# Performance work log

Measured on AMD Instinct MI355X. Metric: run time of the kernel, lower is better.

Reference implementation:

```python
import jax, jax.numpy as jnp
import numpy as np

N_USERS = 100000
M_ITEMS = 200000
K_DIM = 128
N_BASKET = 50
GAMMA = (1.0, 1.0, 1.0, 1.0)


def setup_inputs() -> dict:
    key = jax.random.key(0)
    k1, k2, k3, k4, k5 = jax.random.split(key, 5)
    n, m, k = N_USERS, M_ITEMS, K_DIM
    p = n + 2 * m
    # Build one transaction x of length 2*p: [target transaction t | t^m transaction]
    rng = np.random.default_rng(0)
    x = np.zeros(2 * p, dtype=np.float32)
    # target transaction t
    x[rng.integers(n)] = 1.0                      # user one-hot
    x[n + rng.integers(m)] = 1.0                  # target item one-hot
    basket = rng.choice(m, size=N_BASKET, replace=False)
    x[n + m + basket] = 1.0                       # basket multi-hot
    # t^m transaction (unused by forward math, present for faithfulness)
    x[p + rng.integers(n)] = 1.0
    x[p + n + rng.integers(m)] = 1.0
    basket2 = rng.choice(m, size=N_BASKET, replace=False)
    x[p + n + m + basket2] = 1.0
    return {
        "x": jnp.asarray(x),
        "delta": jnp.ones((1,), dtype=jnp.float32),
        "pmi": jnp.zeros((1,), dtype=jnp.float32),
        "w_0": jax.random.normal(k1, (1,), dtype=jnp.float32),
        "w_bias": jax.random.normal(k2, (p, 1), dtype=jnp.float32),
        "u_V": jax.random.normal(k3, (n, k), dtype=jnp.float32),
        "t_V": jax.random.normal(k4, (m, k), dtype=jnp.float32),
        "b_V": jax.random.normal(k5, (m, k), dtype=jnp.float32),
    }


def _fm(t, w_0, w_bias, u_V, t_V, b_V):
    n, m = u_V.shape[0], t_V.shape[0]
    xr = t[None, :]                                  # (1, n+2m)
    bias = xr @ w_bias                               # (1, 1)
    u_vec = xr[:, :n] @ u_V                          # (1, k) user latent
    t_vec = xr[:, n:n + m] @ t_V                     # (1, k) target-item latent
    xb = t[n + m:]                                   # (m,) basket multi-hot mask
    s = xb @ b_V                                     # (k,)  sum of selected basket vecs
    sq_sum = jnp.sum(xb @ (b_V * b_V))               # scalar sum_i ||b_i||^2
    u_t = jnp.sum(u_vec * t_vec, axis=-1, keepdims=True)   # (1,1)
    t_b = jnp.sum(t_vec * s, axis=-1, keepdims=True)        # (1,1) sum_i t.b_i
    # closed-form FM pairwise trick: sum_{i<j} b_i.b_j = 0.5*(||sum||^2 - sum ||.||^2)
    bs = 0.5 * (jnp.sum(s * s) - sq_sum)                    # scalar
    u_b = jnp.sum(u_vec * s, axis=-1, keepdims=True)        # (1,1)
    g0, g1, g2, g3 = GAMMA
    return w_0 + bias + g0 * u_t + g1 * t_b + g2 * bs + g3 * u_b


def reference(x, delta, pmi, w_0, w_bias, u_V, t_V, b_V):
    n, m = u_V.shape[0], t_V.shape[0]
    p = n + 2 * m
    t = x[:p]
    y = _fm(t, w_0, w_bias, u_V, t_V, b_V)           # (1,1)
    y = -jax.nn.log_sigmoid(y * delta)
    return y
```

## Files before the change

### kernel.cpp

```cpp
#include <hip/hip_runtime.h>
#include <math.h>

#define N_USERS 100000
#define M_ITEMS 200000
#define K_DIM   128
#define P_DIM   (N_USERS + 2 * M_ITEMS)
#define N4      (P_DIM / 4)
#define SCAN_T  256
#define SCAN_BLOCKS ((N4 + SCAN_T - 1) / SCAN_T)
#define SLOTS   64
#define MAXNZ   256


__global__ __launch_bounds__(SCAN_T) void scan_kernel(
        const float* __restrict__ x,
        int* __restrict__ counts,
        int* __restrict__ gidx,
        float* __restrict__ gval) {
    __shared__ int lc;
    __shared__ int   lidx[SLOTS];
    __shared__ float lval[SLOTS];
    const int tid = threadIdx.x;
    const int b   = blockIdx.x;
    if (tid == 0) lc = 0;
    __syncthreads();

    const int i4 = b * SCAN_T + tid;
    if (i4 < N4) {
        float4 v = reinterpret_cast<const float4*>(x)[i4];
        float a[4] = {v.x, v.y, v.z, v.w};
        #pragma unroll
        for (int j = 0; j < 4; ++j) {
            if (a[j] != 0.0f) {
                int p = atomicAdd(&lc, 1);
                if (p < SLOTS) { lidx[p] = 4 * i4 + j; lval[p] = a[j]; }
            }
        }
    }
    __syncthreads();
    int c = lc; if (c > SLOTS) c = SLOTS;
    if (tid == 0) counts[b] = c;
    if (tid < c) {
        gidx[b * SLOTS + tid] = lidx[tid];
        gval[b * SLOTS + tid] = lval[tid];
    }
}

__global__ __launch_bounds__(1024) void finish_kernel(
        const int* __restrict__ counts,
        const int* __restrict__ gidx,
        const float* __restrict__ gval,
        const float* __restrict__ w0,
        const float* __restrict__ delta,
        const float* __restrict__ w_bias,
        const float* __restrict__ uV,
        const float* __restrict__ tV,
        const float* __restrict__ bV,
        float* __restrict__ out) {
    const int tid = threadIdx.x;

    __shared__ int   lcnt;
    __shared__ int   lidx[MAXNZ];
    __shared__ float lval[MAXNZ];
    __shared__ float sb[MAXNZ];
    __shared__ float pu[8][K_DIM], pt[8][K_DIM], ps[8][K_DIM], psq[8][K_DIM];
    __shared__ float red[5][K_DIM];

    if (tid == 0) lcnt = 0;
    __syncthreads();

    if (tid < SCAN_BLOCKS) {
        int cb = counts[tid];
        for (int j = 0; j < cb; ++j) {
            int p = atomicAdd(&lcnt, 1);
            if (p < MAXNZ) {
                lidx[p] = gidx[tid * SLOTS + j];
                lval[p] = gval[tid * SLOTS + j];
            }
        }
    }
    __syncthreads();
    int cnt = lcnt; if (cnt > MAXNZ) cnt = MAXNZ;

    if (tid < MAXNZ)
        sb[tid] = (tid < cnt) ? lval[tid] * w_bias[lidx[tid]] : 0.0f;

    const int k  = tid & (K_DIM - 1);
    const int sl = tid >> 7;
    float u = 0.0f, t = 0.0f, s = 0.0f, sq = 0.0f;
    for (int e = sl; e < cnt; e += 8) {
        const int   idx = lidx[e];
        const float val = lval[e];
        if (idx < N_USERS) {
            u += val * uV[(size_t)idx * K_DIM + k];
        } else if (idx < N_USERS + M_ITEMS) {
            t += val * tV[(size_t)(idx - N_USERS) * K_DIM + k];
        } else {
            float b = bV[(size_t)(idx - N_USERS - M_ITEMS) * K_DIM + k];
            s  += val * b;
            sq += val * b * b;
        }
    }
    pu[sl][k] = u; pt[sl][k] = t; ps[sl][k] = s; psq[sl][k] = sq;
    __syncthreads();

    if (tid < K_DIM) {
        float U = 0.0f, T = 0.0f, S = 0.0f, SQ = 0.0f;
        #pragma unroll
        for (int j = 0; j < 8; ++j) {
            U += pu[j][tid]; T += pt[j][tid]; S += ps[j][tid]; SQ += psq[j][tid];
        }
        red[0][tid] = U * T;
        red[1][tid] = T * S;
        red[2][tid] = S * S;
        red[3][tid] = U * S;
        red[4][tid] = SQ;
    }
    __syncthreads();
    if (tid < 128) sb[tid] += sb[tid + 128];
    __syncthreads();
    for (int off = K_DIM / 2; off > 0; off >>= 1) {
        if (tid < off) {
            #pragma unroll
            for (int j = 0; j < 5; ++j) red[j][tid] += red[j][tid + off];
            sb[tid] += sb[tid + off];
        }
        __syncthreads();
    }

    if (tid == 0) {
        const float ut = red[0][0], tb = red[1][0], ss = red[2][0],
                    ub = red[3][0], sqs = red[4][0];
        const float bs = 0.5f * (ss - sqs);
        float y = w0[0] + sb[0] + ut + tb + bs + ub;
        float z = y * delta[0];
        float a = -z;
        out[0] = fmaxf(a, 0.0f) + log1pf(expf(-fabsf(a)));
    }
}

extern "C" void kernel_launch(void* const* d_in, const int* in_sizes, int n_in,
                              void* d_out, int out_size, void* d_ws, size_t ws_size,
                              hipStream_t stream) {
    const float* x      = (const float*)d_in[0];
    const float* delta  = (const float*)d_in[1];
    const float* w0     = (const float*)d_in[3];
    const float* w_bias = (const float*)d_in[4];
    const float* uV     = (const float*)d_in[5];
    const float* tV     = (const float*)d_in[6];
    const float* bV     = (const float*)d_in[7];
    float* out = (float*)d_out;

    int*   counts = (int*)d_ws;
    int*   gidx   = (int*)((char*)d_ws + 4096);
    float* gval   = (float*)((char*)d_ws + 4096 + SCAN_BLOCKS * SLOTS * sizeof(int));

    scan_kernel<<<SCAN_BLOCKS, SCAN_T, 0, stream>>>(x, counts, gidx, gval);
    finish_kernel<<<1, 1024, 0, stream>>>(counts, gidx, gval, w0, delta,
                                          w_bias, uV, tV, bV, out);
}
```

Before: 206.9 us.

## Fuse scan and finish kernels via last-block ticket and batch row loads

Merges the two launches into one kernel: each 1024-thread block compacts its nonzeros, then an atomic ticket picks the last block to finish, which does the gather and reduction. The scan block size grows from 256 to 1024 threads, so there are fewer per-block slot lists to merge, and MAXNZ shrinks to 128. The gather loop now issues up to 16 row loads per thread up front before accumulating, to expose memory-level parallelism. This removes a kernel launch and the gap between launches. In exchange it relies on a persistent global ticket taken modulo the block count, and the fixed 16-per-slice and 128-entry caps limit how many nonzeros it can handle.

```diff
diff --git a/kernel.cpp b/kernel.cpp
--- a/kernel.cpp
+++ b/kernel.cpp
@@ -6,26 +6,43 @@
 #define K_DIM   128
 #define P_DIM   (N_USERS + 2 * M_ITEMS)
 #define N4      (P_DIM / 4)
-#define SCAN_T  256
-#define SCAN_BLOCKS ((N4 + SCAN_T - 1) / SCAN_T)
+#define BLK     1024
+#define NBLK    ((N4 + BLK - 1) / BLK)
 #define SLOTS   64
-#define MAXNZ   256
+#define MAXNZ   128
 
 
-__global__ __launch_bounds__(SCAN_T) void scan_kernel(
+__device__ unsigned int g_ticket;
+
+__global__ __launch_bounds__(BLK) void fused_kernel(
         const float* __restrict__ x,
-        int* __restrict__ counts,
-        int* __restrict__ gidx,
-        float* __restrict__ gval) {
-    __shared__ int lc;
+        int*   __restrict__ counts,
+        int*   __restrict__ gidx,
+        float* __restrict__ gval,
+        const float* __restrict__ w0,
+        const float* __restrict__ delta,
+        const float* __restrict__ w_bias,
+        const float* __restrict__ uV,
+        const float* __restrict__ tV,
+        const float* __restrict__ bV,
+        float* __restrict__ out) {
+    __shared__ int   lc;
     __shared__ int   lidx[SLOTS];
     __shared__ float lval[SLOTS];
+    __shared__ int   is_last;
+    __shared__ int   lcnt;
+    __shared__ int   fidx[MAXNZ];
+    __shared__ float fval[MAXNZ];
+    __shared__ float sb[MAXNZ];
+    __shared__ float pu[8][K_DIM], pt[8][K_DIM], ps[8][K_DIM], psq[8][K_DIM];
+    __shared__ float red[5][K_DIM];
+
     const int tid = threadIdx.x;
     const int b   = blockIdx.x;
     if (tid == 0) lc = 0;
     __syncthreads();
 
-    const int i4 = b * SCAN_T + tid;
+    const int i4 = b * BLK + tid;
     if (i4 < N4) {
         float4 v = reinterpret_cast<const float4*>(x)[i4];
         float a[4] = {v.x, v.y, v.z, v.w};
@@ -44,38 +61,24 @@
         gidx[b * SLOTS + tid] = lidx[tid];
         gval[b * SLOTS + tid] = lval[tid];
     }
-}
 
-__global__ __launch_bounds__(1024) void finish_kernel(
-        const int* __restrict__ counts,
-        const int* __restrict__ gidx,
-        const float* __restrict__ gval,
-        const float* __restrict__ w0,
-        const float* __restrict__ delta,
-        const float* __restrict__ w_bias,
-        const float* __restrict__ uV,
-        const float* __restrict__ tV,
-        const float* __restrict__ bV,
-        float* __restrict__ out) {
-    const int tid = threadIdx.x;
+    __threadfence();
+    if (tid == 0) {
+        unsigned int old = atomicAdd(&g_ticket, 1u);
+        is_last = ((old % NBLK) == (NBLK - 1)) ? 1 : 0;
+        lcnt = 0;
+    }
+    __syncthreads();
+    if (!is_last) return;
+    __threadfence();
 
-    __shared__ int   lcnt;
-    __shared__ int   lidx[MAXNZ];
-    __shared__ float lval[MAXNZ];
-    __shared__ float sb[MAXNZ];
-    __shared__ float pu[8][K_DIM], pt[8][K_DIM], ps[8][K_DIM], psq[8][K_DIM];
-    __shared__ float red[5][K_DIM];
-
-    if (tid == 0) lcnt = 0;
-    __syncthreads();
-
-    if (tid < SCAN_BLOCKS) {
+    if (tid < NBLK) {
         int cb = counts[tid];
         for (int j = 0; j < cb; ++j) {
             int p = atomicAdd(&lcnt, 1);
             if (p < MAXNZ) {
-                lidx[p] = gidx[tid * SLOTS + j];
-                lval[p] = gval[tid * SLOTS + j];
+                fidx[p] = gidx[tid * SLOTS + j];
+                fval[p] = gval[tid * SLOTS + j];
             }
         }
     }
@@ -83,23 +86,37 @@
     int cnt = lcnt; if (cnt > MAXNZ) cnt = MAXNZ;
 
     if (tid < MAXNZ)
-        sb[tid] = (tid < cnt) ? lval[tid] * w_bias[lidx[tid]] : 0.0f;
+        sb[tid] = (tid < cnt) ? fval[tid] * w_bias[fidx[tid]] : 0.0f;
 
     const int k  = tid & (K_DIM - 1);
     const int sl = tid >> 7;
+    float rows[16], vls[16];
+    int   cl[16];
+    #pragma unroll
+    for (int j = 0; j < 16; ++j) {
+        rows[j] = 0.0f; vls[j] = 0.0f; cl[j] = 3;
+        const int e = sl + 8 * j;
+        if (e < cnt) {
+            const int idx = fidx[e];
+            vls[j] = fval[e];
+            const float* src;
+            if (idx < N_USERS) {
+                src = uV + (size_t)idx * K_DIM;                     cl[j] = 0;
+            } else if (idx < N_USERS + M_ITEMS) {
+                src = tV + (size_t)(idx - N_USERS) * K_DIM;         cl[j] = 1;
+            } else {
+                src = bV + (size_t)(idx - N_USERS - M_ITEMS) * K_DIM; cl[j] = 2;
+            }
+            rows[j] = src[k];
+        }
+    }
     float u = 0.0f, t = 0.0f, s = 0.0f, sq = 0.0f;
-    for (int e = sl; e < cnt; e += 8) {
-        const int   idx = lidx[e];
-        const float val = lval[e];
-        if (idx < N_USERS) {
-            u += val * uV[(size_t)idx * K_DIM + k];
-        } else if (idx < N_USERS + M_ITEMS) {
-            t += val * tV[(size_t)(idx - N_USERS) * K_DIM + k];
-        } else {
-            float b = bV[(size_t)(idx - N_USERS - M_ITEMS) * K_DIM + k];
-            s  += val * b;
-            sq += val * b * b;
-        }
+    #pragma unroll
+    for (int j = 0; j < 16; ++j) {
+        const float vr = vls[j] * rows[j];
+        if      (cl[j] == 0) u += vr;
+        else if (cl[j] == 1) t += vr;
+        else if (cl[j] == 2) { s += vr; sq += vr * rows[j]; }
     }
     pu[sl][k] = u; pt[sl][k] = t; ps[sl][k] = s; psq[sl][k] = sq;
     __syncthreads();
@@ -116,8 +133,6 @@
         red[3][tid] = U * S;
         red[4][tid] = SQ;
     }
-    __syncthreads();
-    if (tid < 128) sb[tid] += sb[tid + 128];
     __syncthreads();
     for (int off = K_DIM / 2; off > 0; off >>= 1) {
         if (tid < off) {
@@ -153,9 +168,8 @@
 
     int*   counts = (int*)d_ws;
     int*   gidx   = (int*)((char*)d_ws + 4096);
-    float* gval   = (float*)((char*)d_ws + 4096 + SCAN_BLOCKS * SLOTS * sizeof(int));
+    float* gval   = (float*)((char*)d_ws + 4096 + NBLK * SLOTS * sizeof(int));
 
-    scan_kernel<<<SCAN_BLOCKS, SCAN_T, 0, stream>>>(x, counts, gidx, gval);
-    finish_kernel<<<1, 1024, 0, stream>>>(counts, gidx, gval, w0, delta,
-                                          w_bias, uV, tV, bV, out);
+    fused_kernel<<<NBLK, BLK, 0, stream>>>(x, counts, gidx, gval,
+                                           w0, delta, w_bias, uV, tV, bV, out);
 }
```

New measurement: 239.0 us. +15.5%, slower.
